# Optimization experiments

Measured on AMD Instinct MI355X. Metric: run time of the kernel, lower is better.

The kernel has to match this reference:

```python
import jax, jax.numpy as jnp
import numpy as np
import math

NUM_IN_C = 128      # rep_2d num_c (c_z)
ATT_C = 64          # attention_num_c
NUM_HEADS = 4
B, T, I, J = 1, 4, 256, 256


def setup_inputs() -> dict:
    key = jax.random.key(0)
    ks = jax.random.split(key, 7)
    s = 1.0 / math.sqrt(NUM_IN_C)
    return {
        "z2d": jax.random.normal(ks[0], (B, I, J, NUM_IN_C), dtype=jnp.float32),
        "t2d": jax.random.normal(ks[1], (B, T, I, J, NUM_IN_C), dtype=jnp.float32),
        # nn.Linear weights are [out_features, in_features]; apply as x @ W.T
        "Wq": jax.random.normal(ks[2], (ATT_C * NUM_HEADS, NUM_IN_C), dtype=jnp.float32) * s,
        "Wk": jax.random.normal(ks[3], (ATT_C * NUM_HEADS, NUM_IN_C), dtype=jnp.float32) * s,
        "Wv": jax.random.normal(ks[4], (ATT_C * NUM_HEADS, NUM_IN_C), dtype=jnp.float32) * s,
        "Wo": jax.random.normal(ks[5], (NUM_IN_C, ATT_C * NUM_HEADS), dtype=jnp.float32) * s,
        "bo": jax.random.normal(ks[6], (NUM_IN_C,), dtype=jnp.float32) * 0.02,
    }


def reference(z2d, t2d, Wq, Wk, Wv, Wo, bo):
    # Projections; reshape last dim to (attention_num_c, num_heads) per torch .view
    q = (z2d @ Wq.T).reshape(*z2d.shape[:-1], ATT_C, NUM_HEADS)        # b i j c h
    k = (t2d @ Wk.T).reshape(*t2d.shape[:-1], ATT_C, NUM_HEADS)        # b t i j c h
    v = (t2d @ Wv.T).reshape(*t2d.shape[:-1], ATT_C, NUM_HEADS)        # b t i j c h
    # NOTE: original scales by sqrt(num_in_c), not sqrt(attention_num_c)
    scores = jnp.einsum('bijch,btijch->btijh', q, k) / math.sqrt(NUM_IN_C)
    w = jax.nn.softmax(scores, axis=1)                                  # softmax over template axis t
    out = jnp.einsum('btijh,btijch->bijch', w, v)                       # b i j c h
    out = out.reshape(*out.shape[:-2], ATT_C * NUM_HEADS)               # flatten (c,h)
    return out @ Wo.T + bo
```

## Files before the change

### kernel.cpp

```cpp
#include <hip/hip_runtime.h>


#define PIX 65536
#define MT 16

typedef __attribute__((ext_vector_type(8))) short s8v;
typedef __attribute__((ext_vector_type(4))) float f4v;
typedef __attribute__((ext_vector_type(4))) unsigned short us4v;
typedef __attribute__((ext_vector_type(4))) float fl4;

__device__ __forceinline__ unsigned short f2bf(float x) {
    unsigned int u = __float_as_uint(x);
    u = (u + 0x7FFFu + ((u >> 16) & 1u)) >> 16;
    return (unsigned short)u;
}
__device__ __forceinline__ float bf2fs(short v) {
    return __uint_as_float(((unsigned int)(unsigned short)v) << 16);
}

__global__ __launch_bounds__(256) void build_weights(
        const float* __restrict__ Wq, const float* __restrict__ Wk,
        const float* __restrict__ Wv, const float* __restrict__ Wo,
        unsigned short* __restrict__ mcat, unsigned short* __restrict__ pcat) {
    int b = blockIdx.x;
    if (b < 256) {
        int idx = b * 256 + threadIdx.x;
        int n = idx >> 7, k1 = idx & 127;
        int h = n >> 7, k2 = n & 127;
        float s = 0.f;
        #pragma unroll 8
        for (int c = 0; c < 64; c++) {
            int r = c * 4 + h;
            s += Wq[r * 128 + k1] * Wk[r * 128 + k2];
        }
        mcat[idx] = f2bf(s * 0.088388347648318447f);
    } else {
        int idx = (b - 256) * 256 + threadIdx.x;
        int m = idx >> 9, kk = idx & 511;
        int h = kk >> 7, k = kk & 127;
        float s = 0.f;
        #pragma unroll 8
        for (int c = 0; c < 64; c++) {
            int r = c * 4 + h;
            s += Wo[m * 256 + r] * Wv[r * 128 + k];
        }
        pcat[idx] = f2bf(s);
    }
}

#define AT_OFS 0
#define U_OFS  8704
#define BUF_USH (8704 + 8384)

__global__ __launch_bounds__(256, 4) void fused_attn(
    const float* __restrict__ z2d, const float* __restrict__ t2d,
    const unsigned short* __restrict__ mcat, const unsigned short* __restrict__ pcat,
    const float* __restrict__ bo, float* __restrict__ out) {

    __shared__ unsigned short buf[BUF_USH];
    __shared__ float Sc[4][16][4];

    const int tid = threadIdx.x;
    const int pbase = blockIdx.x * MT;
    const int wv = tid >> 6, lane = tid & 63, quad = lane >> 4, l15 = lane & 15;

    s8v za[4];
    {
        const float* zp = z2d + (size_t)(pbase + l15) * 128 + quad * 8;
        #pragma unroll
        for (int ks = 0; ks < 4; ks++) {
            const fl4 d0 = *(const fl4*)(zp + ks * 32);
            const fl4 d1 = *(const fl4*)(zp + ks * 32 + 4);
            s8v a;
            a[0] = (short)f2bf(d0[0]); a[1] = (short)f2bf(d0[1]);
            a[2] = (short)f2bf(d0[2]); a[3] = (short)f2bf(d0[3]);
            a[4] = (short)f2bf(d1[0]); a[5] = (short)f2bf(d1[1]);
            a[6] = (short)f2bf(d1[2]); a[7] = (short)f2bf(d1[3]);
            za[ks] = a;
        }
    }

    #pragma unroll
    for (int i = 0; i < 8; i++) {
        int v = i * 256 + tid;
        int t = v >> 9, rem = v & 511, p = rem >> 5, k4 = (rem & 31) << 2;
        const fl4 d = *(const fl4*)(t2d + ((size_t)t * PIX + pbase + p) * 128 + k4);
        us4v w;
        w[0] = f2bf(d[0]); w[1] = f2bf(d[1]); w[2] = f2bf(d[2]); w[3] = f2bf(d[3]);
        *(us4v*)&buf[AT_OFS + (t * 16 + p) * 136 + k4] = w;
    }
    __syncthreads();

    #pragma unroll
    for (int cb = 0; cb < 8; cb++) {
        const int col = wv * 128 + cb * 16 + l15;
        s8v b[4];
        #pragma unroll
        for (int ks = 0; ks < 4; ks++)
            b[ks] = *(const s8v*)(mcat + (size_t)col * 128 + ks * 32 + quad * 8);
        f4v acc = {0.f, 0.f, 0.f, 0.f};
        #pragma unroll
        for (int ks = 0; ks < 4; ks++)
            acc = __builtin_amdgcn_mfma_f32_16x16x32_bf16(za[ks], b[ks], acc, 0, 0, 0);
        #pragma unroll
        for (int r = 0; r < 4; r++)
            buf[U_OFS + (quad * 4 + r) * 524 + col] = f2bf(acc[r]);
    }
    __syncthreads();

    {
        const int t = wv;
        s8v bt[4];
        #pragma unroll
        for (int ks = 0; ks < 4; ks++)
            bt[ks] = *(const s8v*)&buf[AT_OFS + (t * 16 + l15) * 136 + ks * 32 + quad * 8];
        #pragma unroll
        for (int h = 0; h < 4; h++) {
            f4v c = {0.f, 0.f, 0.f, 0.f};
            #pragma unroll
            for (int ks = 0; ks < 4; ks++) {
                const s8v a = *(const s8v*)&buf[U_OFS + l15 * 524
                                                 + h * 128 + ks * 32 + quad * 8];
                c = __builtin_amdgcn_mfma_f32_16x16x32_bf16(a, bt[ks], c, 0, 0, 0);
            }
            const int rsel = l15 & 3;
            float dv = rsel == 0 ? c[0] : rsel == 1 ? c[1] : rsel == 2 ? c[2] : c[3];
            if ((l15 >> 2) == quad) Sc[t][l15][h] = dv;
        }
    }
    __syncthreads();

    if (tid < 64) {
        const int p = tid >> 2, h = tid & 3;
        float x0 = Sc[0][p][h], x1 = Sc[1][p][h], x2 = Sc[2][p][h], x3 = Sc[3][p][h];
        float mx = fmaxf(fmaxf(x0, x1), fmaxf(x2, x3));
        float e0 = __expf(x0 - mx), e1 = __expf(x1 - mx);
        float e2 = __expf(x2 - mx), e3 = __expf(x3 - mx);
        float inv = 1.f / (e0 + e1 + e2 + e3);
        Sc[0][p][h] = e0 * inv; Sc[1][p][h] = e1 * inv;
        Sc[2][p][h] = e2 * inv; Sc[3][p][h] = e3 * inv;
    }
    __syncthreads();

    {
        const int p = tid >> 4, seg = tid & 15, k = seg * 8;
        float w[4][4];
        #pragma unroll
        for (int t = 0; t < 4; t++) {
            const fl4 ww = *(const fl4*)&Sc[t][p][0];
            w[t][0] = ww[0]; w[t][1] = ww[1]; w[t][2] = ww[2]; w[t][3] = ww[3];
        }
        s8v a[4];
        #pragma unroll
        for (int t = 0; t < 4; t++)
            a[t] = *(const s8v*)&buf[AT_OFS + (t * 16 + p) * 136 + k];
        s8v o[4];
        #pragma unroll
        for (int j = 0; j < 8; j++) {
            const float a0 = bf2fs(a[0][j]), a1 = bf2fs(a[1][j]);
            const float a2 = bf2fs(a[2][j]), a3 = bf2fs(a[3][j]);
            #pragma unroll
            for (int h = 0; h < 4; h++) {
                o[h][j] = (short)f2bf(w[0][h] * a0 + w[1][h] * a1
                                    + w[2][h] * a2 + w[3][h] * a3);
            }
        }
        #pragma unroll
        for (int h = 0; h < 4; h++)
            *(s8v*)&buf[AT_OFS + (h * 16 + p) * 136 + k] = o[h];
    }
    __syncthreads();

    f4v accd[2];
    accd[0] = (f4v){0.f, 0.f, 0.f, 0.f};
    accd[1] = (f4v){0.f, 0.f, 0.f, 0.f};
    #pragma unroll
    for (int h = 0; h < 4; h++) {
        s8v af[4];
        #pragma unroll
        for (int ks = 0; ks < 4; ks++)
            af[ks] = *(const s8v*)&buf[AT_OFS + (h * 16 + l15) * 136 + ks * 32 + quad * 8];
        #pragma unroll
        for (int nt = 0; nt < 2; nt++) {
            #pragma unroll
            for (int ks = 0; ks < 4; ks++) {
                const s8v b = *(const s8v*)(pcat + (size_t)(wv * 32 + nt * 16 + l15) * 512
                                                 + h * 128 + ks * 32 + quad * 8);
                accd[nt] = __builtin_amdgcn_mfma_f32_16x16x32_bf16(af[ks], b, accd[nt], 0, 0, 0);
            }
        }
    }

    #pragma unroll
    for (int nt = 0; nt < 2; nt++) {
        const int m = wv * 32 + nt * 16 + l15;
        const float bb = bo[m];
        #pragma unroll
        for (int r = 0; r < 4; r++) {
            out[(size_t)(pbase + quad * 4 + r) * 128 + m] = accd[nt][r] + bb;
        }
    }
}

extern "C" void kernel_launch(void* const* d_in, const int* in_sizes, int n_in,
                              void* d_out, int out_size, void* d_ws, size_t ws_size,
                              hipStream_t stream) {
    const float* z2d = (const float*)d_in[0];
    const float* t2d = (const float*)d_in[1];
    const float* Wq  = (const float*)d_in[2];
    const float* Wk  = (const float*)d_in[3];
    const float* Wv  = (const float*)d_in[4];
    const float* Wo  = (const float*)d_in[5];
    const float* bo  = (const float*)d_in[6];

    unsigned short* mcat = (unsigned short*)d_ws;
    unsigned short* pcat = mcat + 512 * 128;

    build_weights<<<512, 256, 0, stream>>>(Wq, Wk, Wv, Wo, mcat, pcat);
    fused_attn<<<PIX / MT, 256, 0, stream>>>(z2d, t2d, mcat, pcat, bo, (float*)d_out);
}
```

Before: 325.2 us.

## Split fused attention into score and output kernels with LDS-resident weights

The single fused kernel, which re-read the folded weight matrices from global memory for every 16-pixel tile, is replaced by two persistent-style kernels of 256 blocks × 512 threads. Each kernel first stages its whole bf16 weight matrix (mcat or pcat) in LDS and then loops over many pixel tiles. The score kernel computes softmax weights per wave using a small per-wave scratch and writes them to a global workspace. The output kernel re-reads t2d, mixes it per head and runs the output projection. The split removes repeated weight fetches and block-wide barriers, at the cost of reading t2d twice, an extra weight round-trip through global memory, and large LDS use per block.

Result: faster. 277.3 us (-14.7%).

```diff
diff --git a/kernel.cpp b/kernel.cpp
--- a/kernel.cpp
+++ b/kernel.cpp
@@ -2,11 +2,10 @@
 
 
 #define PIX 65536
-#define MT 16
 
 typedef __attribute__((ext_vector_type(8))) short s8v;
 typedef __attribute__((ext_vector_type(4))) float f4v;
-typedef __attribute__((ext_vector_type(4))) unsigned short us4v;
+typedef __attribute__((ext_vector_type(4))) unsigned int u4v;
 typedef __attribute__((ext_vector_type(4))) float fl4;
 
 __device__ __forceinline__ unsigned short f2bf(float x) {
@@ -48,157 +47,205 @@
     }
 }
 
-#define AT_OFS 0
-#define U_OFS  8704
-#define BUF_USH (8704 + 8384)
-
-__global__ __launch_bounds__(256, 4) void fused_attn(
+#define S_SCR_OFS (512 * 136)
+#define S_USH (S_SCR_OFS + 8 * 16 * 72)
+
+__global__ __launch_bounds__(512, 2) void score_kernel(
     const float* __restrict__ z2d, const float* __restrict__ t2d,
-    const unsigned short* __restrict__ mcat, const unsigned short* __restrict__ pcat,
-    const float* __restrict__ bo, float* __restrict__ out) {
-
-    __shared__ unsigned short buf[BUF_USH];
-    __shared__ float Sc[4][16][4];
-
+    const unsigned short* __restrict__ mcat, float* __restrict__ wbuf) {
+
+    __shared__ unsigned short sm[S_USH];
     const int tid = threadIdx.x;
-    const int pbase = blockIdx.x * MT;
+
+    #pragma unroll
+    for (int i = 0; i < 16; i++) {
+        int g8 = i * 512 + tid;
+        int row = g8 >> 4, c8 = g8 & 15;
+        *(u4v*)&sm[row * 136 + c8 * 8] = *(const u4v*)(mcat + (size_t)g8 * 8);
+    }
+    __syncthreads();
+
     const int wv = tid >> 6, lane = tid & 63, quad = lane >> 4, l15 = lane & 15;
-
-    s8v za[4];
-    {
-        const float* zp = z2d + (size_t)(pbase + l15) * 128 + quad * 8;
-        #pragma unroll
-        for (int ks = 0; ks < 4; ks++) {
-            const fl4 d0 = *(const fl4*)(zp + ks * 32);
-            const fl4 d1 = *(const fl4*)(zp + ks * 32 + 4);
-            s8v a;
-            a[0] = (short)f2bf(d0[0]); a[1] = (short)f2bf(d0[1]);
-            a[2] = (short)f2bf(d0[2]); a[3] = (short)f2bf(d0[3]);
-            a[4] = (short)f2bf(d1[0]); a[5] = (short)f2bf(d1[1]);
-            a[6] = (short)f2bf(d1[2]); a[7] = (short)f2bf(d1[3]);
-            za[ks] = a;
-        }
-    }
-
-    #pragma unroll
-    for (int i = 0; i < 8; i++) {
-        int v = i * 256 + tid;
-        int t = v >> 9, rem = v & 511, p = rem >> 5, k4 = (rem & 31) << 2;
-        const fl4 d = *(const fl4*)(t2d + ((size_t)t * PIX + pbase + p) * 128 + k4);
-        us4v w;
-        w[0] = f2bf(d[0]); w[1] = f2bf(d[1]); w[2] = f2bf(d[2]); w[3] = f2bf(d[3]);
-        *(us4v*)&buf[AT_OFS + (t * 16 + p) * 136 + k4] = w;
+    unsigned short* scr = &sm[S_SCR_OFS + wv * (16 * 72)];
+
+    for (int it = 0; it < 2; it++) {
+        const int p0 = blockIdx.x * 256 + (wv * 2 + it) * 16;
+
+        s8v za[4];
+        {
+            const float* zp = z2d + (size_t)(p0 + l15) * 128 + quad * 8;
+            #pragma unroll
+            for (int ks = 0; ks < 4; ks++) {
+                const fl4 d0 = *(const fl4*)(zp + ks * 32);
+                const fl4 d1 = *(const fl4*)(zp + ks * 32 + 4);
+                s8v a;
+                a[0] = (short)f2bf(d0[0]); a[1] = (short)f2bf(d0[1]);
+                a[2] = (short)f2bf(d0[2]); a[3] = (short)f2bf(d0[3]);
+                a[4] = (short)f2bf(d1[0]); a[5] = (short)f2bf(d1[1]);
+                a[6] = (short)f2bf(d1[2]); a[7] = (short)f2bf(d1[3]);
+                za[ks] = a;
+            }
+        }
+        s8v atf[4][4];
+        #pragma unroll
+        for (int t = 0; t < 4; t++) {
+            const float* ap = t2d + ((size_t)t * PIX + p0 + l15) * 128 + quad * 8;
+            #pragma unroll
+            for (int kf = 0; kf < 4; kf++) {
+                const fl4 d0 = *(const fl4*)(ap + kf * 32);
+                const fl4 d1 = *(const fl4*)(ap + kf * 32 + 4);
+                s8v a;
+                a[0] = (short)f2bf(d0[0]); a[1] = (short)f2bf(d0[1]);
+                a[2] = (short)f2bf(d0[2]); a[3] = (short)f2bf(d0[3]);
+                a[4] = (short)f2bf(d1[0]); a[5] = (short)f2bf(d1[1]);
+                a[6] = (short)f2bf(d1[2]); a[7] = (short)f2bf(d1[3]);
+                atf[t][kf] = a;
+            }
+        }
+
+        for (int h = 0; h < 4; h++) {
+            f4v dac[4];
+            #pragma unroll
+            for (int t = 0; t < 4; t++) dac[t] = (f4v){0.f, 0.f, 0.f, 0.f};
+
+            #pragma unroll
+            for (int ph = 0; ph < 2; ph++) {
+                f4v uacc[4];
+                #pragma unroll
+                for (int c = 0; c < 4; c++) {
+                    const int brow = h * 128 + (ph * 4 + c) * 16 + l15;
+                    f4v acc = {0.f, 0.f, 0.f, 0.f};
+                    #pragma unroll
+                    for (int ks = 0; ks < 4; ks++) {
+                        const s8v b = *(const s8v*)&sm[brow * 136 + ks * 32 + quad * 8];
+                        acc = __builtin_amdgcn_mfma_f32_16x16x32_bf16(za[ks], b, acc, 0, 0, 0);
+                    }
+                    uacc[c] = acc;
+                }
+                #pragma unroll
+                for (int c = 0; c < 4; c++)
+                    #pragma unroll
+                    for (int r = 0; r < 4; r++)
+                        scr[(quad * 4 + r) * 72 + c * 16 + l15] = f2bf(uacc[c][r]);
+                __threadfence_block();
+                #pragma unroll
+                for (int ks2 = 0; ks2 < 2; ks2++) {
+                    const s8v uf = *(const s8v*)&scr[l15 * 72 + ks2 * 32 + quad * 8];
+                    const int kf = ph * 2 + ks2;
+                    #pragma unroll
+                    for (int t = 0; t < 4; t++)
+                        dac[t] = __builtin_amdgcn_mfma_f32_16x16x32_bf16(
+                            uf, atf[t][kf], dac[t], 0, 0, 0);
+                }
+                __threadfence_block();
+            }
+            if ((l15 >> 2) == quad) {
+                const int r = l15 & 3;
+                float x0 = r == 0 ? dac[0][0] : r == 1 ? dac[0][1] : r == 2 ? dac[0][2] : dac[0][3];
+                float x1 = r == 0 ? dac[1][0] : r == 1 ? dac[1][1] : r == 2 ? dac[1][2] : dac[1][3];
+                float x2 = r == 0 ? dac[2][0] : r == 1 ? dac[2][1] : r == 2 ? dac[2][2] : dac[2][3];
+                float x3 = r == 0 ? dac[3][0] : r == 1 ? dac[3][1] : r == 2 ? dac[3][2] : dac[3][3];
+                float mx = fmaxf(fmaxf(x0, x1), fmaxf(x2, x3));
+                float e0 = __expf(x0 - mx), e1 = __expf(x1 - mx);
+                float e2 = __expf(x2 - mx), e3 = __expf(x3 - mx);
+                float inv = 1.f / (e0 + e1 + e2 + e3);
+                float* wp = wbuf + (size_t)h * 4 * PIX + p0 + l15;
+                wp[0 * PIX] = e0 * inv; wp[1 * PIX] = e1 * inv;
+                wp[2 * PIX] = e2 * inv; wp[3 * PIX] = e3 * inv;
+            }
+        }
+    }
+}
+
+#define O_USH (128 * 520)
+
+__global__ __launch_bounds__(512, 2) void out_kernel(
+    const float* __restrict__ t2d, const unsigned short* __restrict__ pcat,
+    const float* __restrict__ wbuf, const float* __restrict__ bo,
+    float* __restrict__ out) {
+
+    __shared__ unsigned short sm[O_USH];
+    const int tid = threadIdx.x;
+
+    #pragma unroll
+    for (int i = 0; i < 16; i++) {
+        int g8 = i * 512 + tid;
+        int row = g8 >> 6, c8 = g8 & 63;
+        *(u4v*)&sm[row * 520 + c8 * 8] = *(const u4v*)(pcat + (size_t)g8 * 8);
     }
     __syncthreads();
 
-    #pragma unroll
-    for (int cb = 0; cb < 8; cb++) {
-        const int col = wv * 128 + cb * 16 + l15;
-        s8v b[4];
-        #pragma unroll
-        for (int ks = 0; ks < 4; ks++)
-            b[ks] = *(const s8v*)(mcat + (size_t)col * 128 + ks * 32 + quad * 8);
-        f4v acc = {0.f, 0.f, 0.f, 0.f};
-        #pragma unroll
-        for (int ks = 0; ks < 4; ks++)
-            acc = __builtin_amdgcn_mfma_f32_16x16x32_bf16(za[ks], b[ks], acc, 0, 0, 0);
-        #pragma unroll
-        for (int r = 0; r < 4; r++)
-            buf[U_OFS + (quad * 4 + r) * 524 + col] = f2bf(acc[r]);
-    }
-    __syncthreads();
-
-    {
-        const int t = wv;
-        s8v bt[4];
-        #pragma unroll
-        for (int ks = 0; ks < 4; ks++)
-            bt[ks] = *(const s8v*)&buf[AT_OFS + (t * 16 + l15) * 136 + ks * 32 + quad * 8];
+    const int wv = tid >> 6, lane = tid & 63, quad = lane >> 4, l15 = lane & 15;
+    const int p0 = blockIdx.x * 256 + wv * 32;
+
+    float wgt[4][2][4];
+    #pragma unroll
+    for (int h = 0; h < 4; h++)
+        #pragma unroll
+        for (int t = 0; t < 4; t++)
+            #pragma unroll
+            for (int mt = 0; mt < 2; mt++)
+                wgt[t][mt][h] = wbuf[(size_t)(h * 4 + t) * PIX + p0 + mt * 16 + l15];
+
+    f4v acc[2][8];
+    #pragma unroll
+    for (int mt = 0; mt < 2; mt++)
+        #pragma unroll
+        for (int ct = 0; ct < 8; ct++) acc[mt][ct] = (f4v){0.f, 0.f, 0.f, 0.f};
+
+    #pragma unroll
+    for (int ks = 0; ks < 4; ks++) {
+        s8v ab[4][2];
+        #pragma unroll
+        for (int t = 0; t < 4; t++)
+            #pragma unroll
+            for (int mt = 0; mt < 2; mt++) {
+                const float* ap = t2d + ((size_t)t * PIX + p0 + mt * 16 + l15) * 128
+                                  + ks * 32 + quad * 8;
+                const fl4 d0 = *(const fl4*)ap;
+                const fl4 d1 = *(const fl4*)(ap + 4);
+                s8v a;
+                a[0] = (short)f2bf(d0[0]); a[1] = (short)f2bf(d0[1]);
+                a[2] = (short)f2bf(d0[2]); a[3] = (short)f2bf(d0[3]);
+                a[4] = (short)f2bf(d1[0]); a[5] = (short)f2bf(d1[1]);
+                a[6] = (short)f2bf(d1[2]); a[7] = (short)f2bf(d1[3]);
+                ab[t][mt] = a;
+            }
         #pragma unroll
         for (int h = 0; h < 4; h++) {
-            f4v c = {0.f, 0.f, 0.f, 0.f};
-            #pragma unroll
-            for (int ks = 0; ks < 4; ks++) {
-                const s8v a = *(const s8v*)&buf[U_OFS + l15 * 524
-                                                 + h * 128 + ks * 32 + quad * 8];
-                c = __builtin_amdgcn_mfma_f32_16x16x32_bf16(a, bt[ks], c, 0, 0, 0);
-            }
-            const int rsel = l15 & 3;
-            float dv = rsel == 0 ? c[0] : rsel == 1 ? c[1] : rsel == 2 ? c[2] : c[3];
-            if ((l15 >> 2) == quad) Sc[t][l15][h] = dv;
-        }
-    }
-    __syncthreads();
-
-    if (tid < 64) {
-        const int p = tid >> 2, h = tid & 3;
-        float x0 = Sc[0][p][h], x1 = Sc[1][p][h], x2 = Sc[2][p][h], x3 = Sc[3][p][h];
-        float mx = fmaxf(fmaxf(x0, x1), fmaxf(x2, x3));
-        float e0 = __expf(x0 - mx), e1 = __expf(x1 - mx);
-        float e2 = __expf(x2 - mx), e3 = __expf(x3 - mx);
-        float inv = 1.f / (e0 + e1 + e2 + e3);
-        Sc[0][p][h] = e0 * inv; Sc[1][p][h] = e1 * inv;
-        Sc[2][p][h] = e2 * inv; Sc[3][p][h] = e3 * inv;
-    }
-    __syncthreads();
-
-    {
-        const int p = tid >> 4, seg = tid & 15, k = seg * 8;
-        float w[4][4];
-        #pragma unroll
-        for (int t = 0; t < 4; t++) {
-            const fl4 ww = *(const fl4*)&Sc[t][p][0];
-            w[t][0] = ww[0]; w[t][1] = ww[1]; w[t][2] = ww[2]; w[t][3] = ww[3];
-        }
-        s8v a[4];
-        #pragma unroll
-        for (int t = 0; t < 4; t++)
-            a[t] = *(const s8v*)&buf[AT_OFS + (t * 16 + p) * 136 + k];
-        s8v o[4];
-        #pragma unroll
-        for (int j = 0; j < 8; j++) {
-            const float a0 = bf2fs(a[0][j]), a1 = bf2fs(a[1][j]);
-            const float a2 = bf2fs(a[2][j]), a3 = bf2fs(a[3][j]);
-            #pragma unroll
-            for (int h = 0; h < 4; h++) {
-                o[h][j] = (short)f2bf(w[0][h] * a0 + w[1][h] * a1
-                                    + w[2][h] * a2 + w[3][h] * a3);
-            }
-        }
-        #pragma unroll
-        for (int h = 0; h < 4; h++)
-            *(s8v*)&buf[AT_OFS + (h * 16 + p) * 136 + k] = o[h];
-    }
-    __syncthreads();
-
-    f4v accd[2];
-    accd[0] = (f4v){0.f, 0.f, 0.f, 0.f};
-    accd[1] = (f4v){0.f, 0.f, 0.f, 0.f};
-    #pragma unroll
-    for (int h = 0; h < 4; h++) {
-        s8v af[4];
-        #pragma unroll
-        for (int ks = 0; ks < 4; ks++)
-            af[ks] = *(const s8v*)&buf[AT_OFS + (h * 16 + l15) * 136 + ks * 32 + quad * 8];
-        #pragma unroll
-        for (int nt = 0; nt < 2; nt++) {
-            #pragma unroll
-            for (int ks = 0; ks < 4; ks++) {
-                const s8v b = *(const s8v*)(pcat + (size_t)(wv * 32 + nt * 16 + l15) * 512
-                                                 + h * 128 + ks * 32 + quad * 8);
-                accd[nt] = __builtin_amdgcn_mfma_f32_16x16x32_bf16(af[ks], b, accd[nt], 0, 0, 0);
-            }
-        }
-    }
-
-    #pragma unroll
-    for (int nt = 0; nt < 2; nt++) {
-        const int m = wv * 32 + nt * 16 + l15;
-        const float bb = bo[m];
-        #pragma unroll
-        for (int r = 0; r < 4; r++) {
-            out[(size_t)(pbase + quad * 4 + r) * 128 + m] = accd[nt][r] + bb;
-        }
+            s8v af[2];
+            #pragma unroll
+            for (int mt = 0; mt < 2; mt++) {
+                s8v o;
+                #pragma unroll
+                for (int j = 0; j < 8; j++) {
+                    float v = wgt[0][mt][h] * bf2fs(ab[0][mt][j])
+                            + wgt[1][mt][h] * bf2fs(ab[1][mt][j])
+                            + wgt[2][mt][h] * bf2fs(ab[2][mt][j])
+                            + wgt[3][mt][h] * bf2fs(ab[3][mt][j]);
+                    o[j] = (short)f2bf(v);
+                }
+                af[mt] = o;
+            }
+            #pragma unroll
+            for (int ct = 0; ct < 8; ct++) {
+                const s8v b = *(const s8v*)&sm[(ct * 16 + l15) * 520
+                                               + h * 128 + ks * 32 + quad * 8];
+                acc[0][ct] = __builtin_amdgcn_mfma_f32_16x16x32_bf16(af[0], b, acc[0][ct], 0, 0, 0);
+                acc[1][ct] = __builtin_amdgcn_mfma_f32_16x16x32_bf16(af[1], b, acc[1][ct], 0, 0, 0);
+            }
+        }
+    }
+
+    #pragma unroll
+    for (int ct = 0; ct < 8; ct++) {
+        const float bb = bo[ct * 16 + l15];
+        #pragma unroll
+        for (int mt = 0; mt < 2; mt++)
+            #pragma unroll
+            for (int r = 0; r < 4; r++)
+                out[(size_t)(p0 + mt * 16 + quad * 4 + r) * 128 + ct * 16 + l15]
+                    = acc[mt][ct][r] + bb;
     }
 }
 
@@ -215,7 +262,9 @@
 
     unsigned short* mcat = (unsigned short*)d_ws;
     unsigned short* pcat = mcat + 512 * 128;
+    float* wbuf = (float*)(pcat + 128 * 512);
 
     build_weights<<<512, 256, 0, stream>>>(Wq, Wk, Wv, Wo, mcat, pcat);
-    fused_attn<<<PIX / MT, 256, 0, stream>>>(z2d, t2d, mcat, pcat, bo, (float*)d_out);
-}
+    score_kernel<<<256, 512, 0, stream>>>(z2d, t2d, mcat, wbuf);
+    out_kernel<<<256, 512, 0, stream>>>(t2d, pcat, wbuf, bo, (float*)d_out);
+}
```
